# Kernel tuning notes

Measured on AMD Instinct MI355X. Metric: run time of the kernel, lower is better.

Reference implementation:

```python
import jax, jax.numpy as jnp
import numpy as np

EPS = 1e-5
N_NODES = 10
NUM_JOINTS = 6   # all robot_configs fixed to '3_segments_3DOF' (module's fallback default)
MAX_DOF = 10


def _lin(x, w, b):
    # torch nn.Linear: y = x @ W.T + b, W is (out, in)
    return jnp.einsum('...i,oi->...o', x, w) + b


def _layernorm(x, scale, bias):
    mu = x.mean(-1, keepdims=True)
    var = x.var(-1, keepdims=True)
    return (x - mu) / jnp.sqrt(var + EPS) * scale + bias


def _forward(images, text_lengths, node_features, edge_indices, p):
    B = images.shape[0]
    # --- SimplifiedVLMBackbone ---
    y = jax.lax.conv_general_dilated(images, p['conv_w'], (2, 2), [(3, 3), (3, 3)],
                                     dimension_numbers=('NCHW', 'OIHW', 'NCHW'))
    y = jax.nn.relu(y + p['conv_b'][None, :, None, None])          # (B,32,112,112)
    y = y.reshape(B, 32, 7, 16, 7, 16).mean(axis=(3, 5))            # adaptive avg pool -> (B,32,7,7)
    y = y.reshape(B, 32 * 49)
    y = jax.nn.relu(_lin(y, p['img_fc1_w'], p['img_fc1_b']))
    img_feat = _lin(y, p['img_fc2_w'], p['img_fc2_b'])               # (B,768)
    t = p['text_emb'][jnp.clip(text_lengths, 0, 9999)]               # (B,256)
    vlm = img_feat + _lin(t, p['text_fc_w'], p['text_fc_b'])         # (B,768)

    # --- SoftArmGraphNN ---
    x = jax.nn.relu(_lin(node_features, p['enc1_w'], p['enc1_b']))
    x = _lin(x, p['enc2_w'], p['enc2_b'])                            # (B,N,64)
    src, dst = edge_indices[:, 0, :], edge_indices[:, 1, :]          # (B,E)

    def agg_fn(xi, si, di):
        # mean of neighbor (source) features per destination node; 0 if no neighbors
        g = xi[si]                                                   # (E,D)
        s = jax.ops.segment_sum(g, di, num_segments=N_NODES)
        c = jax.ops.segment_sum(jnp.ones(di.shape, xi.dtype), di, num_segments=N_NODES)
        return s / jnp.maximum(c, 1.0)[:, None]

    for i in range(3):
        residual = x
        mean_nb = jax.vmap(agg_fn)(x, src, dst)                      # (B,N,64)
        comb = jnp.concatenate([x, mean_nb], axis=-1)                # (B,N,128)
        x = _lin(comb, p['gc_w'][i], p['gc_b'][i])
        x = jax.nn.relu(_layernorm(x + residual, p['ln_scale'][i], p['ln_bias'][i]))
    graph_tokens = _lin(x, p['proj_w'], p['proj_b'])                 # (B,N,32)

    # --- AttentionPooling + dual-path fusion ---
    s = _lin(jnp.tanh(_lin(graph_tokens, p['attn1_w'], p['attn1_b'])), p['attn2_w'], p['attn2_b'])
    w = jax.nn.softmax(s, axis=1)                                    # (B,N,1)
    robot_token = jnp.sum(graph_tokens * w, axis=1)                  # (B,32) -> project? 32 vs 768 -> residual add via broadcast pad
    fused = vlm.at[:, :robot_token.shape[-1]].add(robot_token)       # global token residual into vlm features

    # --- NodeActionHead (all samples: 3seg_3DOF -> 6 joints, per-joint MLPs) ---
    comb = jnp.concatenate([
        jnp.broadcast_to(fused[:, None, :], (B, NUM_JOINTS, fused.shape[-1])),
        graph_tokens[:, :NUM_JOINTS, :]], axis=-1)                   # (B,J,800)
    h = jax.nn.relu(jnp.einsum('bjf,jhf->bjh', comb, p['head_w1']) + p['head_b1'])
    h = jax.nn.relu(jnp.einsum('bjf,jhf->bjh', h, p['head_w2']) + p['head_b2'])
    a = jnp.einsum('bjf,jhf->bjh', h, p['head_w3']) + p['head_b3']   # (B,6,16)
    a = jnp.pad(a, ((0, 0), (0, MAX_DOF - NUM_JOINTS), (0, 0)))      # pad to max_dof
    return jnp.transpose(a, (0, 2, 1))                               # (B,16,10)


def setup_inputs() -> dict:
    key = jax.random.key(0)
    ks = iter(jax.random.split(key, 64))

    def nrm(shape, scale=0.02):
        return scale * jax.random.normal(next(ks), shape, dtype=jnp.float32)

    B = 128
    inp = {
        'images': jax.random.normal(next(ks), (B, 3, 224, 224), dtype=jnp.float32),
        'text_lengths': jax.random.randint(next(ks), (B,), 0, 10000, dtype=jnp.int32),
        'node_features': jax.random.normal(next(ks), (B, N_NODES, 19), dtype=jnp.float32),
        'edge_indices': jax.random.randint(next(ks), (B, 2, 18), 0, N_NODES, dtype=jnp.int32),
        'conv_w': nrm((32, 3, 7, 7)), 'conv_b': jnp.zeros(32, jnp.float32),
        'img_fc1_w': nrm((512, 1568)), 'img_fc1_b': jnp.zeros(512, jnp.float32),
        'img_fc2_w': nrm((768, 512)), 'img_fc2_b': jnp.zeros(768, jnp.float32),
        'text_emb': nrm((10000, 256)),
        'text_fc_w': nrm((768, 256)), 'text_fc_b': jnp.zeros(768, jnp.float32),
        'enc1_w': nrm((64, 19)), 'enc1_b': jnp.zeros(64, jnp.float32),
        'enc2_w': nrm((64, 64)), 'enc2_b': jnp.zeros(64, jnp.float32),
        'gc_w': nrm((3, 64, 128)), 'gc_b': jnp.zeros((3, 64), jnp.float32),
        'ln_scale': jnp.ones((3, 64), jnp.float32), 'ln_bias': jnp.zeros((3, 64), jnp.float32),
        'proj_w': nrm((32, 64)), 'proj_b': jnp.zeros(32, jnp.float32),
        'attn1_w': nrm((16, 32)), 'attn1_b': jnp.zeros(16, jnp.float32),
        'attn2_w': nrm((1, 16)), 'attn2_b': jnp.zeros(1, jnp.float32),
        'head_w1': nrm((6, 128, 800)), 'head_b1': jnp.zeros((6, 128), jnp.float32),
        'head_w2': nrm((6, 64, 128)), 'head_b2': jnp.zeros((6, 64), jnp.float32),
        'head_w3': nrm((6, 16, 64)), 'head_b3': jnp.zeros((6, 16), jnp.float32),
    }
    return inp


def reference(images, text_lengths, node_features, edge_indices, conv_w, conv_b,
              img_fc1_w, img_fc1_b, img_fc2_w, img_fc2_b, text_emb, text_fc_w, text_fc_b,
              enc1_w, enc1_b, enc2_w, enc2_b, gc_w, gc_b, ln_scale, ln_bias,
              proj_w, proj_b, attn1_w, attn1_b, attn2_w, attn2_b,
              head_w1, head_b1, head_w2, head_b2, head_w3, head_b3):
    p = dict(conv_w=conv_w, conv_b=conv_b, img_fc1_w=img_fc1_w, img_fc1_b=img_fc1_b,
             img_fc2_w=img_fc2_w, img_fc2_b=img_fc2_b, text_emb=text_emb,
             text_fc_w=text_fc_w, text_fc_b=text_fc_b, enc1_w=enc1_w, enc1_b=enc1_b,
             enc2_w=enc2_w, enc2_b=enc2_b, gc_w=gc_w, gc_b=gc_b, ln_scale=ln_scale,
             ln_bias=ln_bias, proj_w=proj_w, proj_b=proj_b, attn1_w=attn1_w,
             attn1_b=attn1_b, attn2_w=attn2_w, attn2_b=attn2_b, head_w1=head_w1,
             head_b1=head_b1, head_w2=head_w2, head_b2=head_b2, head_w3=head_w3,
             head_b3=head_b3)
    return _forward(images, text_lengths, node_features, edge_indices, p)
```

## Files before the change

### kernel.cpp

```cpp
#include <hip/hip_runtime.h>
#include <hip/hip_bf16.h>
#include <math.h>

typedef __attribute__((ext_vector_type(8))) short bf16x8;
typedef __attribute__((ext_vector_type(4))) float f32x4;

static __device__ __forceinline__ unsigned short f2bf(float f) {
    union { float f; unsigned int u; } x{f};
    unsigned int u = x.u;
    unsigned int r = (u + 0x7fffu + ((u >> 16) & 1u)) >> 16;
    return (unsigned short)r;
}

static __device__ __forceinline__ unsigned int pack2(float f0, float f1) {
    __hip_bfloat162 h = __float22bfloat162_rn(float2{f0, f1});
    union { __hip_bfloat162 h; unsigned int u; } c{h};
    return c.u;
}

__global__ __launch_bounds__(256) void wprep(const float* __restrict__ conv_w,
                                             unsigned short* __restrict__ wB) {
    for (int idx = threadIdx.x; idx < 24 * 32 * 8; idx += 256) {
        int s = idx >> 8;
        int ch = (idx >> 3) & 31;
        int kx = idx & 7;
        int c = s >> 3, ky = s & 7;
        float v = 0.f;
        if (ky < 7 && kx < 7) v = conv_w[ch * 147 + c * 49 + ky * 7 + kx];
        wB[idx] = f2bf(v);
    }
}

#define PSTRIDE 120
__global__ __launch_bounds__(512, 4) void conv_mfma(const float* __restrict__ img,
                                                    const unsigned int* __restrict__ wBu,
                                                    const float* __restrict__ cb,
                                                    float* __restrict__ pooled) {
    __shared__ unsigned int patch[111 * PSTRIDE];
    const int t = threadIdx.x;
    const int py = blockIdx.x, b = blockIdx.y;
    const int lane = t & 63, wid = t >> 6;
    const int r16 = lane & 15, g = lane >> 4;
    const int Y0 = 32 * py - 3;

    const int xc0 = 2 * lane - 3;
    const int xc1 = 2 * lane + 125;
    const int a00 = max(xc0, 0);
    const int a01 = max(xc0 + 1, 0);
    const int a10 = min(xc1, 223);
    const int a11 = min(xc1 + 1, 223);
    const bool v00 = (xc0 >= 0);
    const bool v01 = (xc0 + 1 >= 0);
    const bool v10 = (xc1 <= 223);
    const bool v11 = (xc1 + 1 <= 223);
    const bool c1act = (lane < 52);

    const float* ib = img + (size_t)b * 3 * 224 * 224;

#pragma unroll
    for (int hb = 0; hb < 2; ++hb) {
        float g0[7], g1[7], g2[7], g3[7];
        int rr[7];
        bool rv[7];
#pragma unroll
        for (int i = 0; i < 7; ++i) {
            int r = wid + 8 * (hb * 7 + i);
            int c_ = (r >= 74) ? 2 : ((r >= 37) ? 1 : 0);
            int pr = r - 37 * c_;
            int iy = Y0 + pr;
            rv[i] = (r < 111) & (iy >= 0) & (iy < 224);
            int iyc = min(max(iy, 0), 223);
            const float* rp = ib + (c_ * 224 + iyc) * 224;
            rr[i] = r;
            g0[i] = rp[a00];
            g1[i] = rp[a01];
            g2[i] = rp[a10];
            g3[i] = rp[a11];
        }
#pragma unroll
        for (int i = 0; i < 7; ++i) {
            float f0 = (rv[i] && v00) ? g0[i] : 0.f;
            float f1 = (rv[i] && v01) ? g1[i] : 0.f;
            float f2_ = (rv[i] && v10) ? g2[i] : 0.f;
            float f3 = (rv[i] && v11) ? g3[i] : 0.f;
            if (rr[i] < 111) {
                patch[rr[i] * PSTRIDE + lane] = pack2(f0, f1);
                if (c1act) patch[rr[i] * PSTRIDE + 64 + lane] = pack2(f2_, f3);
            }
        }
    }

    bf16x8 bfrA[6], bfrB[6];
    int rowoff[6];
#pragma unroll
    for (int k = 0; k < 6; ++k) {
        int s = 4 * k + g;
        int c = s >> 3, ky = s & 7;
        int kyc = ky > 6 ? 6 : ky;
        rowoff[k] = c * 37 + kyc;
        union { uint4 q; bf16x8 v; } ua, ub;
        ua.q = *(const uint4*)(wBu + (s * 32 + r16) * 4);
        ub.q = *(const uint4*)(wBu + (s * 32 + r16 + 16) * 4);
        bfrA[k] = ua.v;
        bfrB[k] = ub.v;
    }
    const float biasA = cb[r16], biasB = cb[r16 + 16];

    __syncthreads();

    float accA[7], accB[7];
#pragma unroll
    for (int p = 0; p < 7; ++p) accA[p] = accB[p] = 0.f;

#pragma unroll
    for (int q = 0; q < 2; ++q) {
        const int oyl = 2 * wid + q;
        int rb[6];
#pragma unroll
        for (int k = 0; k < 6; ++k) rb[k] = (rowoff[k] + 2 * oyl) * PSTRIDE;

        for (int t7 = 0; t7 < 7; ++t7) {
            const int oxr = 16 * t7 + r16;
            f32x4 C0 = {biasA, biasA, biasA, biasA};
            f32x4 C1 = {biasB, biasB, biasB, biasB};
#pragma unroll
            for (int k = 0; k < 6; ++k) {
                const unsigned int* ap = &patch[rb[k] + oxr];
                union { unsigned int u[4]; bf16x8 v; } ua;
                ua.u[0] = ap[0];
                ua.u[1] = ap[1];
                ua.u[2] = ap[2];
                ua.u[3] = ap[3];
                C0 = __builtin_amdgcn_mfma_f32_16x16x32_bf16(ua.v, bfrA[k], C0, 0, 0, 0);
                C1 = __builtin_amdgcn_mfma_f32_16x16x32_bf16(ua.v, bfrB[k], C1, 0, 0, 0);
            }
            float s0 = 0.f, s1 = 0.f;
#pragma unroll
            for (int r = 0; r < 4; ++r) {
                s0 += fmaxf(C0[r], 0.f);
                s1 += fmaxf(C1[r], 0.f);
            }
            accA[t7] += s0;
            accB[t7] += s1;
        }
    }
#pragma unroll
    for (int p = 0; p < 7; ++p) {
        accA[p] += __shfl_xor(accA[p], 16);
        accA[p] += __shfl_xor(accA[p], 32);
        accB[p] += __shfl_xor(accB[p], 16);
        accB[p] += __shfl_xor(accB[p], 32);
    }
    __syncthreads();
    float* sw = (float*)patch;
    if (lane < 16) {
#pragma unroll
        for (int p = 0; p < 7; ++p) {
            sw[(wid * 7 + p) * 32 + lane] = accA[p];
            sw[(wid * 7 + p) * 32 + lane + 16] = accB[p];
        }
    }
    __syncthreads();
    if (t < 224) {
        int p = t >> 5, ch = t & 31;
        float s = 0.f;
#pragma unroll
        for (int w = 0; w < 8; ++w) s += sw[(w * 7 + p) * 32 + ch];
        pooled[(size_t)b * 1568 + ch * 49 + py * 7 + p] = s * (1.f / 256.f);
    }
}

__global__ __launch_bounds__(256) void fc1_k(const float* __restrict__ in,
                                             const float* __restrict__ w,
                                             const float* __restrict__ bias,
                                             float* __restrict__ out) {
    const int t = threadIdx.x, lane = t & 63, wid = t >> 6;
    const int qg = blockIdx.x & 31;
    const int bg = blockIdx.x >> 5;
    const int b0 = bg * 8;
    const int o0 = (qg * 4 + wid) * 4;
    const float4* wp = (const float4*)w;
    const float4* xp = (const float4*)in;

    float acc[4][8];
#pragma unroll
    for (int oo = 0; oo < 4; ++oo)
#pragma unroll
        for (int r = 0; r < 8; ++r) acc[oo][r] = 0.f;

    for (int i = lane; i < 392; i += 64) {
        float4 wv[4];
#pragma unroll
        for (int oo = 0; oo < 4; ++oo) wv[oo] = wp[(size_t)(o0 + oo) * 392 + i];
#pragma unroll
        for (int r = 0; r < 8; ++r) {
            float4 xv = xp[(size_t)(b0 + r) * 392 + i];
#pragma unroll
            for (int oo = 0; oo < 4; ++oo) {
                acc[oo][r] = fmaf(xv.x, wv[oo].x, acc[oo][r]);
                acc[oo][r] = fmaf(xv.y, wv[oo].y, acc[oo][r]);
                acc[oo][r] = fmaf(xv.z, wv[oo].z, acc[oo][r]);
                acc[oo][r] = fmaf(xv.w, wv[oo].w, acc[oo][r]);
            }
        }
    }
#pragma unroll
    for (int oo = 0; oo < 4; ++oo) {
        float v = 0.f;
#pragma unroll
        for (int r = 0; r < 8; ++r) {
            float s = acc[oo][r];
            s += __shfl_xor(s, 32);
            s += __shfl_xor(s, 16);
            s += __shfl_xor(s, 8);
            s += __shfl_xor(s, 4);
            s += __shfl_xor(s, 2);
            s += __shfl_xor(s, 1);
            if (lane == r) v = s;
        }
        if (lane < 8)
            out[(size_t)(b0 + lane) * 512 + o0 + oo] = fmaxf(v + bias[o0 + oo], 0.f);
    }
}

__global__ __launch_bounds__(256) void vlm_k(const float* __restrict__ h1,
                                             const float* __restrict__ w2,
                                             const float* __restrict__ b2,
                                             const int* __restrict__ tlen,
                                             const float* __restrict__ temb,
                                             const float* __restrict__ tw,
                                             const float* __restrict__ tb,
                                             const float* __restrict__ rtok,
                                             float* __restrict__ fused) {
    const int t = threadIdx.x, lane = t & 63, wid = t >> 6;
    const int ogq = blockIdx.x % 48;
    const int bg = blockIdx.x / 48;
    const int b0 = bg * 8;
    const int o0 = (ogq * 4 + wid) * 4;

    int rows[8];
#pragma unroll
    for (int r = 0; r < 8; ++r) {
        int v = tlen[b0 + r];
        rows[r] = min(max(v, 0), 9999);
    }
    const float4* wp = (const float4*)w2;
    const float4* xp = (const float4*)h1;
    const float4* wtp = (const float4*)tw;
    const float4* xtp = (const float4*)temb;

    float acc[4][8];
#pragma unroll
    for (int oo = 0; oo < 4; ++oo)
#pragma unroll
        for (int r = 0; r < 8; ++r) acc[oo][r] = 0.f;

#pragma unroll
    for (int ii = 0; ii < 2; ++ii) {
        int i = lane + (ii << 6);
        float4 wv[4];
#pragma unroll
        for (int oo = 0; oo < 4; ++oo) wv[oo] = wp[(size_t)(o0 + oo) * 128 + i];
#pragma unroll
        for (int r = 0; r < 8; ++r) {
            float4 xv = xp[(size_t)(b0 + r) * 128 + i];
#pragma unroll
            for (int oo = 0; oo < 4; ++oo) {
                acc[oo][r] = fmaf(xv.x, wv[oo].x, acc[oo][r]);
                acc[oo][r] = fmaf(xv.y, wv[oo].y, acc[oo][r]);
                acc[oo][r] = fmaf(xv.z, wv[oo].z, acc[oo][r]);
                acc[oo][r] = fmaf(xv.w, wv[oo].w, acc[oo][r]);
            }
        }
    }
    {
        float4 wv[4];
#pragma unroll
        for (int oo = 0; oo < 4; ++oo) wv[oo] = wtp[(size_t)(o0 + oo) * 64 + lane];
#pragma unroll
        for (int r = 0; r < 8; ++r) {
            float4 xv = xtp[(size_t)rows[r] * 64 + lane];
#pragma unroll
            for (int oo = 0; oo < 4; ++oo) {
                acc[oo][r] = fmaf(xv.x, wv[oo].x, acc[oo][r]);
                acc[oo][r] = fmaf(xv.y, wv[oo].y, acc[oo][r]);
                acc[oo][r] = fmaf(xv.z, wv[oo].z, acc[oo][r]);
                acc[oo][r] = fmaf(xv.w, wv[oo].w, acc[oo][r]);
            }
        }
    }
#pragma unroll
    for (int oo = 0; oo < 4; ++oo) {
        float v = 0.f;
#pragma unroll
        for (int r = 0; r < 8; ++r) {
            float s = acc[oo][r];
            s += __shfl_xor(s, 32);
            s += __shfl_xor(s, 16);
            s += __shfl_xor(s, 8);
            s += __shfl_xor(s, 4);
            s += __shfl_xor(s, 2);
            s += __shfl_xor(s, 1);
            if (lane == r) v = s;
        }
        int o = o0 + oo;
        if (lane < 8) {
            float add = (o < 32) ? rtok[(size_t)(b0 + lane) * 32 + o] : 0.f;
            fused[(size_t)(b0 + lane) * 768 + o] = v + b2[o] + tb[o] + add;
        }
    }
}

__global__ __launch_bounds__(640, 1) void graph_k(
    const float* __restrict__ nfeat, const int* __restrict__ eidx,
    const float* __restrict__ e1w, const float* __restrict__ e1b,
    const float* __restrict__ e2w, const float* __restrict__ e2b,
    const float* __restrict__ gcw, const float* __restrict__ gcb,
    const float* __restrict__ lns, const float* __restrict__ lnb,
    const float* __restrict__ pjw, const float* __restrict__ pjb,
    const float* __restrict__ a1w, const float* __restrict__ a1b,
    const float* __restrict__ a2w, const float* __restrict__ a2b,
    float* __restrict__ gts_g, float* __restrict__ rtok) {
    __shared__ __align__(16) float pool[8448];
    __shared__ __align__(16) float nf[10][20];
    __shared__ __align__(16) float xsA[10][64];
    __shared__ __align__(16) float xsB[10][64];
    __shared__ __align__(16) float nbs[10][64];
    __shared__ __align__(16) float gtss[10][32];
    __shared__ float svs[10];
    __shared__ int se[18], de[18];
    const int t = threadIdx.x;
    const int b = blockIdx.x;
    const int n = t >> 6, o = t & 63;

    if (t < 190) {
        int nn = t / 19, i = t - nn * 19;
        nf[nn][i] = nfeat[(size_t)(b * 10 + nn) * 19 + i];
    }
    if (t < 36) {
        if (t < 18) se[t] = eidx[b * 36 + t];
        else de[t - 18] = eidx[b * 36 + t];
    }
    float* e1wT = pool;
    float* e2wT = pool + 1280;
    for (int u = t; u < 1216; u += 640) {
        int oo = u / 19, k = u - oo * 19;
        e1wT[k * 64 + oo] = e1w[u];
    }
    for (int u = t; u < 4096; u += 640) {
        int oo = u >> 6, k = u & 63;
        e2wT[k * 65 + oo] = e2w[u];
    }
    __syncthreads();

    {
        float acc = e1b[o];
#pragma unroll
        for (int i = 0; i < 19; ++i) acc = fmaf(nf[n][i], e1wT[i * 64 + o], acc);
        xsB[n][o] = fmaxf(acc, 0.f);
    }
    {
        const float* xrow = &xsB[n][0];
        float s0 = 0, s1 = 0, s2 = 0, s3 = 0;
#pragma unroll
        for (int k = 0; k < 64; k += 4) {
            s0 = fmaf(xrow[k], e2wT[k * 65 + o], s0);
            s1 = fmaf(xrow[k + 1], e2wT[(k + 1) * 65 + o], s1);
            s2 = fmaf(xrow[k + 2], e2wT[(k + 2) * 65 + o], s2);
            s3 = fmaf(xrow[k + 3], e2wT[(k + 3) * 65 + o], s3);
        }
        xsA[n][o] = e2b[o] + ((s0 + s1) + (s2 + s3));
    }
    __syncthreads();

    float* src = &xsA[0][0];
    float* dst = &xsB[0][0];
    for (int l = 0; l < 3; ++l) {
        const float* gl = gcw + (size_t)l * 8192;
        for (int u = t; u < 8192; u += 640) {
            int oo = u >> 7, k = u & 127;
            pool[k * 65 + oo] = gl[u];
        }
        {
            float s = 0.f;
            int cnt = 0;
#pragma unroll
            for (int e = 0; e < 18; ++e) {
                bool m = (de[e] == n);
                float v = src[se[e] * 64 + o];
                s += m ? v : 0.f;
                cnt += m ? 1 : 0;
            }
            nbs[n][o] = s / (float)(cnt > 1 ? cnt : 1);
        }
        __syncthreads();
        {
            const float* xa = src + n * 64;
            const float* xb = &nbs[n][0];
            float s0 = 0, s1 = 0, s2 = 0, s3 = 0;
#pragma unroll
            for (int k = 0; k < 64; k += 4) {
                s0 = fmaf(xa[k], pool[k * 65 + o], s0);
                s1 = fmaf(xa[k + 1], pool[(k + 1) * 65 + o], s1);
                s2 = fmaf(xa[k + 2], pool[(k + 2) * 65 + o], s2);
                s3 = fmaf(xa[k + 3], pool[(k + 3) * 65 + o], s3);
            }
#pragma unroll
            for (int k = 0; k < 64; k += 4) {
                s0 = fmaf(xb[k], pool[(64 + k) * 65 + o], s0);
                s1 = fmaf(xb[k + 1], pool[(64 + k + 1) * 65 + o], s1);
                s2 = fmaf(xb[k + 2], pool[(64 + k + 2) * 65 + o], s2);
                s3 = fmaf(xb[k + 3], pool[(64 + k + 3) * 65 + o], s3);
            }
            float v = gcb[l * 64 + o] + ((s0 + s1) + (s2 + s3)) + xa[o];
            float mu = v;
            mu += __shfl_xor(mu, 32);
            mu += __shfl_xor(mu, 16);
            mu += __shfl_xor(mu, 8);
            mu += __shfl_xor(mu, 4);
            mu += __shfl_xor(mu, 2);
            mu += __shfl_xor(mu, 1);
            mu *= (1.f / 64.f);
            float d = v - mu;
            float vr = d * d;
            vr += __shfl_xor(vr, 32);
            vr += __shfl_xor(vr, 16);
            vr += __shfl_xor(vr, 8);
            vr += __shfl_xor(vr, 4);
            vr += __shfl_xor(vr, 2);
            vr += __shfl_xor(vr, 1);
            vr *= (1.f / 64.f);
            dst[n * 64 + o] =
                fmaxf(d / sqrtf(vr + 1e-5f) * lns[l * 64 + o] + lnb[l * 64 + o], 0.f);
        }
        __syncthreads();
        float* tmp = src;
        src = dst;
        dst = tmp;
    }

    float* pjwT = pool;
    float* a1wT = pool + 2112;
    for (int u = t; u < 2048; u += 640) {
        int oo = u >> 6, k = u & 63;
        pjwT[k * 33 + oo] = pjw[u];
    }
    for (int u = t; u < 512; u += 640) {
        int hh = u >> 5, k = u & 31;
        a1wT[k * 17 + hh] = a1w[u];
    }
    __syncthreads();

    if (o < 32) {
        const float* xrow = src + n * 64;
        float s0 = 0, s1 = 0, s2 = 0, s3 = 0;
#pragma unroll
        for (int k = 0; k < 64; k += 4) {
            s0 = fmaf(xrow[k], pjwT[k * 33 + o], s0);
            s1 = fmaf(xrow[k + 1], pjwT[(k + 1) * 33 + o], s1);
            s2 = fmaf(xrow[k + 2], pjwT[(k + 2) * 33 + o], s2);
            s3 = fmaf(xrow[k + 3], pjwT[(k + 3) * 33 + o], s3);
        }
        float gv = pjb[o] + ((s0 + s1) + (s2 + s3));
        gtss[n][o] = gv;
        gts_g[(size_t)b * 320 + n * 32 + o] = gv;
    }
    if (o < 16) {
        const float* xrow = &gtss[n][0];
        float s0 = 0, s1 = 0, s2 = 0, s3 = 0;
#pragma unroll
        for (int k = 0; k < 32; k += 4) {
            s0 = fmaf(xrow[k], a1wT[k * 17 + o], s0);
            s1 = fmaf(xrow[k + 1], a1wT[(k + 1) * 17 + o], s1);
            s2 = fmaf(xrow[k + 2], a1wT[(k + 2) * 17 + o], s2);
            s3 = fmaf(xrow[k + 3], a1wT[(k + 3) * 17 + o], s3);
        }
        float z = a1b[o] + ((s0 + s1) + (s2 + s3));
        float sc = tanhf(z) * a2w[o];
        sc += __shfl_xor(sc, 8);
        sc += __shfl_xor(sc, 4);
        sc += __shfl_xor(sc, 2);
        sc += __shfl_xor(sc, 1);
        if (o == 0) svs[n] = sc + a2b[0];
    }
    __syncthreads();

    if (n == 0 && o < 32) {
        float m = svs[0];
#pragma unroll
        for (int i = 1; i < 10; ++i) m = fmaxf(m, svs[i]);
        float e[10];
        float sum = 0.f;
#pragma unroll
        for (int i = 0; i < 10; ++i) {
            e[i] = expf(svs[i] - m);
            sum += e[i];
        }
        float inv = 1.f / sum;
        float rt = 0.f;
#pragma unroll
        for (int nn = 0; nn < 10; ++nn) rt = fmaf(gtss[nn][o], e[nn] * inv, rt);
        rtok[(size_t)b * 32 + o] = rt;
    }
}

__global__ __launch_bounds__(256) void head1_k(const float* __restrict__ fused,
                                               const float* __restrict__ gts,
                                               const float* __restrict__ w1,
                                               const float* __restrict__ b1,
                                               float* __restrict__ h1T) {
    const int t = threadIdx.x, lane = t & 63, wid = t >> 6;
    const int ogq = blockIdx.x % 48;
    const int bg = blockIdx.x / 48;
    const int b0 = bg * 8;
    const int j = ogq >> 3;
    const int o0 = ogq * 16 + wid * 4;
    const float4* wp = (const float4*)w1;
    const float4* fp = (const float4*)fused;
    const float4* gp = (const float4*)gts;

    float acc[4][8];
#pragma unroll
    for (int oo = 0; oo < 4; ++oo)
#pragma unroll
        for (int r = 0; r < 8; ++r) acc[oo][r] = 0.f;

    for (int i = lane; i < 200; i += 64) {
        float4 wv[4];
#pragma unroll
        for (int oo = 0; oo < 4; ++oo) wv[oo] = wp[(size_t)(o0 + oo) * 200 + i];
#pragma unroll
        for (int r = 0; r < 8; ++r) {
            float4 xv = (i < 192) ? fp[(size_t)(b0 + r) * 192 + i]
                                  : gp[(size_t)(b0 + r) * 80 + j * 8 + (i - 192)];
#pragma unroll
            for (int oo = 0; oo < 4; ++oo) {
                acc[oo][r] = fmaf(xv.x, wv[oo].x, acc[oo][r]);
                acc[oo][r] = fmaf(xv.y, wv[oo].y, acc[oo][r]);
                acc[oo][r] = fmaf(xv.z, wv[oo].z, acc[oo][r]);
                acc[oo][r] = fmaf(xv.w, wv[oo].w, acc[oo][r]);
            }
        }
    }
#pragma unroll
    for (int oo = 0; oo < 4; ++oo) {
        float v = 0.f;
#pragma unroll
        for (int r = 0; r < 8; ++r) {
            float s = acc[oo][r];
            s += __shfl_xor(s, 32);
            s += __shfl_xor(s, 16);
            s += __shfl_xor(s, 8);
            s += __shfl_xor(s, 4);
            s += __shfl_xor(s, 2);
            s += __shfl_xor(s, 1);
// ... 37 lines not shown
    out[(size_t)b * 160 + oo * 10 + jj] = acc;
}

extern "C" void kernel_launch(void* const* d_in, const int* in_sizes, int n_in,
                              void* d_out, int out_size, void* d_ws, size_t ws_size,
                              hipStream_t stream) {
    const float* images = (const float*)d_in[0];
    const int* tlen = (const int*)d_in[1];
    const float* nfeat = (const float*)d_in[2];
    const int* eidx = (const int*)d_in[3];
    const float* conv_w = (const float*)d_in[4];
    const float* conv_b = (const float*)d_in[5];
    const float* fc1w = (const float*)d_in[6];
    const float* fc1b = (const float*)d_in[7];
    const float* fc2w = (const float*)d_in[8];
    const float* fc2b = (const float*)d_in[9];
    const float* temb = (const float*)d_in[10];
    const float* tfw = (const float*)d_in[11];
    const float* tfb = (const float*)d_in[12];
    const float* e1w = (const float*)d_in[13];
    const float* e1b = (const float*)d_in[14];
    const float* e2w = (const float*)d_in[15];
    const float* e2b = (const float*)d_in[16];
    const float* gcw = (const float*)d_in[17];
    const float* gcb = (const float*)d_in[18];
    const float* lns = (const float*)d_in[19];
    const float* lnb = (const float*)d_in[20];
    const float* pjw = (const float*)d_in[21];
    const float* pjb = (const float*)d_in[22];
    const float* a1w = (const float*)d_in[23];
    const float* a1b = (const float*)d_in[24];
    const float* a2w = (const float*)d_in[25];
    const float* a2b = (const float*)d_in[26];
    const float* w1 = (const float*)d_in[27];
    const float* b1 = (const float*)d_in[28];
    const float* w2 = (const float*)d_in[29];
    const float* b2 = (const float*)d_in[30];
    const float* w3 = (const float*)d_in[31];
    const float* b3 = (const float*)d_in[32];

    const int B = in_sizes[0] / (3 * 224 * 224);

    float* ws = (float*)d_ws;
    unsigned short* wB = (unsigned short*)d_ws;
    float* pooled = ws + 3072;
    float* h1fc = pooled + (size_t)B * 1568;
    float* fused = h1fc + (size_t)B * 512;
    float* gts = fused + (size_t)B * 768;
    float* rtok = gts + (size_t)B * 320;
    float* h1T = pooled;
    float* h2T = pooled + 98304;

    wprep<<<1, 256, 0, stream>>>(conv_w, wB);
    conv_mfma<<<dim3(7, B), 512, 0, stream>>>(images, (const unsigned int*)wB,
                                              conv_b, pooled);
    fc1_k<<<512, 256, 0, stream>>>(pooled, fc1w, fc1b, h1fc);
    graph_k<<<B, 640, 0, stream>>>(nfeat, eidx, e1w, e1b, e2w, e2b, gcw, gcb,
                                   lns, lnb, pjw, pjb, a1w, a1b, a2w, a2b,
                                   gts, rtok);
    vlm_k<<<768, 256, 0, stream>>>(h1fc, fc2w, fc2b, tlen, temb, tfw, tfb,
                                   rtok, fused);
    head1_k<<<768, 256, 0, stream>>>(fused, gts, w1, b1, h1T);
    head2_k<<<384, 128, 0, stream>>>(h1T, w2, b2, h2T);
    head3_k<<<160, 128, 0, stream>>>(h2T, w3, b3, (float*)d_out);
}
```

Measured before the change: 119.9 us.

## Merge graph network kernel into conv kernel as extra block column

The graph network work is folded into the convolution launch as an eighth block per batch row, so a separate kernel launch goes away and the graph work runs alongside the conv blocks. Shared memory is now one union buffer sized for the conv patch, and the graph code is reworked to use 512 threads (8 waves looping over 10 nodes) instead of 640. This saves a launch and overlaps the small graph work with conv, but the graph blocks now run with fewer threads and under the conv kernel's launch bounds.

```diff
diff --git a/kernel.cpp b/kernel.cpp
--- a/kernel.cpp
+++ b/kernel.cpp
@@ -32,286 +32,9 @@
 }
 
 #define PSTRIDE 120
-__global__ __launch_bounds__(512, 4) void conv_mfma(const float* __restrict__ img,
-                                                    const unsigned int* __restrict__ wBu,
-                                                    const float* __restrict__ cb,
-                                                    float* __restrict__ pooled) {
-    __shared__ unsigned int patch[111 * PSTRIDE];
-    const int t = threadIdx.x;
-    const int py = blockIdx.x, b = blockIdx.y;
-    const int lane = t & 63, wid = t >> 6;
-    const int r16 = lane & 15, g = lane >> 4;
-    const int Y0 = 32 * py - 3;
-
-    const int xc0 = 2 * lane - 3;
-    const int xc1 = 2 * lane + 125;
-    const int a00 = max(xc0, 0);
-    const int a01 = max(xc0 + 1, 0);
-    const int a10 = min(xc1, 223);
-    const int a11 = min(xc1 + 1, 223);
-    const bool v00 = (xc0 >= 0);
-    const bool v01 = (xc0 + 1 >= 0);
-    const bool v10 = (xc1 <= 223);
-    const bool v11 = (xc1 + 1 <= 223);
-    const bool c1act = (lane < 52);
-
-    const float* ib = img + (size_t)b * 3 * 224 * 224;
-
-#pragma unroll
-    for (int hb = 0; hb < 2; ++hb) {
-        float g0[7], g1[7], g2[7], g3[7];
-        int rr[7];
-        bool rv[7];
-#pragma unroll
-        for (int i = 0; i < 7; ++i) {
-            int r = wid + 8 * (hb * 7 + i);
-            int c_ = (r >= 74) ? 2 : ((r >= 37) ? 1 : 0);
-            int pr = r - 37 * c_;
-            int iy = Y0 + pr;
-            rv[i] = (r < 111) & (iy >= 0) & (iy < 224);
-            int iyc = min(max(iy, 0), 223);
-            const float* rp = ib + (c_ * 224 + iyc) * 224;
-            rr[i] = r;
-            g0[i] = rp[a00];
-            g1[i] = rp[a01];
-            g2[i] = rp[a10];
-            g3[i] = rp[a11];
-        }
-#pragma unroll
-        for (int i = 0; i < 7; ++i) {
-            float f0 = (rv[i] && v00) ? g0[i] : 0.f;
-            float f1 = (rv[i] && v01) ? g1[i] : 0.f;
-            float f2_ = (rv[i] && v10) ? g2[i] : 0.f;
-            float f3 = (rv[i] && v11) ? g3[i] : 0.f;
-            if (rr[i] < 111) {
-                patch[rr[i] * PSTRIDE + lane] = pack2(f0, f1);
-                if (c1act) patch[rr[i] * PSTRIDE + 64 + lane] = pack2(f2_, f3);
-            }
-        }
-    }
-
-    bf16x8 bfrA[6], bfrB[6];
-    int rowoff[6];
-#pragma unroll
-    for (int k = 0; k < 6; ++k) {
-        int s = 4 * k + g;
-        int c = s >> 3, ky = s & 7;
-        int kyc = ky > 6 ? 6 : ky;
-        rowoff[k] = c * 37 + kyc;
-        union { uint4 q; bf16x8 v; } ua, ub;
-        ua.q = *(const uint4*)(wBu + (s * 32 + r16) * 4);
-        ub.q = *(const uint4*)(wBu + (s * 32 + r16 + 16) * 4);
-        bfrA[k] = ua.v;
-        bfrB[k] = ub.v;
-    }
-    const float biasA = cb[r16], biasB = cb[r16 + 16];
-
-    __syncthreads();
-
-    float accA[7], accB[7];
-#pragma unroll
-    for (int p = 0; p < 7; ++p) accA[p] = accB[p] = 0.f;
-
-#pragma unroll
-    for (int q = 0; q < 2; ++q) {
-        const int oyl = 2 * wid + q;
-        int rb[6];
-#pragma unroll
-        for (int k = 0; k < 6; ++k) rb[k] = (rowoff[k] + 2 * oyl) * PSTRIDE;
-
-        for (int t7 = 0; t7 < 7; ++t7) {
-            const int oxr = 16 * t7 + r16;
-            f32x4 C0 = {biasA, biasA, biasA, biasA};
-            f32x4 C1 = {biasB, biasB, biasB, biasB};
-#pragma unroll
-            for (int k = 0; k < 6; ++k) {
-                const unsigned int* ap = &patch[rb[k] + oxr];
-                union { unsigned int u[4]; bf16x8 v; } ua;
-                ua.u[0] = ap[0];
-                ua.u[1] = ap[1];
-                ua.u[2] = ap[2];
-                ua.u[3] = ap[3];
-                C0 = __builtin_amdgcn_mfma_f32_16x16x32_bf16(ua.v, bfrA[k], C0, 0, 0, 0);
-                C1 = __builtin_amdgcn_mfma_f32_16x16x32_bf16(ua.v, bfrB[k], C1, 0, 0, 0);
-            }
-            float s0 = 0.f, s1 = 0.f;
-#pragma unroll
-            for (int r = 0; r < 4; ++r) {
-                s0 += fmaxf(C0[r], 0.f);
-                s1 += fmaxf(C1[r], 0.f);
-            }
-            accA[t7] += s0;
-            accB[t7] += s1;
-        }
-    }
-#pragma unroll
-    for (int p = 0; p < 7; ++p) {
-        accA[p] += __shfl_xor(accA[p], 16);
-        accA[p] += __shfl_xor(accA[p], 32);
-        accB[p] += __shfl_xor(accB[p], 16);
-        accB[p] += __shfl_xor(accB[p], 32);
-    }
-    __syncthreads();
-    float* sw = (float*)patch;
-    if (lane < 16) {
-#pragma unroll
-        for (int p = 0; p < 7; ++p) {
-            sw[(wid * 7 + p) * 32 + lane] = accA[p];
-            sw[(wid * 7 + p) * 32 + lane + 16] = accB[p];
-        }
-    }
-    __syncthreads();
-    if (t < 224) {
-        int p = t >> 5, ch = t & 31;
-        float s = 0.f;
-#pragma unroll
-        for (int w = 0; w < 8; ++w) s += sw[(w * 7 + p) * 32 + ch];
-        pooled[(size_t)b * 1568 + ch * 49 + py * 7 + p] = s * (1.f / 256.f);
-    }
-}
-
-__global__ __launch_bounds__(256) void fc1_k(const float* __restrict__ in,
-                                             const float* __restrict__ w,
-                                             const float* __restrict__ bias,
-                                             float* __restrict__ out) {
-    const int t = threadIdx.x, lane = t & 63, wid = t >> 6;
-    const int qg = blockIdx.x & 31;
-    const int bg = blockIdx.x >> 5;
-    const int b0 = bg * 8;
-    const int o0 = (qg * 4 + wid) * 4;
-    const float4* wp = (const float4*)w;
-    const float4* xp = (const float4*)in;
-
-    float acc[4][8];
-#pragma unroll
-    for (int oo = 0; oo < 4; ++oo)
-#pragma unroll
-        for (int r = 0; r < 8; ++r) acc[oo][r] = 0.f;
-
-    for (int i = lane; i < 392; i += 64) {
-        float4 wv[4];
-#pragma unroll
-        for (int oo = 0; oo < 4; ++oo) wv[oo] = wp[(size_t)(o0 + oo) * 392 + i];
-#pragma unroll
-        for (int r = 0; r < 8; ++r) {
-            float4 xv = xp[(size_t)(b0 + r) * 392 + i];
-#pragma unroll
-            for (int oo = 0; oo < 4; ++oo) {
-                acc[oo][r] = fmaf(xv.x, wv[oo].x, acc[oo][r]);
-                acc[oo][r] = fmaf(xv.y, wv[oo].y, acc[oo][r]);
-                acc[oo][r] = fmaf(xv.z, wv[oo].z, acc[oo][r]);
-                acc[oo][r] = fmaf(xv.w, wv[oo].w, acc[oo][r]);
-            }
-        }
-    }
-#pragma unroll
-    for (int oo = 0; oo < 4; ++oo) {
-        float v = 0.f;
-#pragma unroll
-        for (int r = 0; r < 8; ++r) {
-            float s = acc[oo][r];
-            s += __shfl_xor(s, 32);
-            s += __shfl_xor(s, 16);
-            s += __shfl_xor(s, 8);
-            s += __shfl_xor(s, 4);
-            s += __shfl_xor(s, 2);
-            s += __shfl_xor(s, 1);
-            if (lane == r) v = s;
-        }
-        if (lane < 8)
-            out[(size_t)(b0 + lane) * 512 + o0 + oo] = fmaxf(v + bias[o0 + oo], 0.f);
-    }
-}
-
-__global__ __launch_bounds__(256) void vlm_k(const float* __restrict__ h1,
-                                             const float* __restrict__ w2,
-                                             const float* __restrict__ b2,
-                                             const int* __restrict__ tlen,
-                                             const float* __restrict__ temb,
-                                             const float* __restrict__ tw,
-                                             const float* __restrict__ tb,
-                                             const float* __restrict__ rtok,
-                                             float* __restrict__ fused) {
-    const int t = threadIdx.x, lane = t & 63, wid = t >> 6;
-    const int ogq = blockIdx.x % 48;
-    const int bg = blockIdx.x / 48;
-    const int b0 = bg * 8;
-    const int o0 = (ogq * 4 + wid) * 4;
-
-    int rows[8];
-#pragma unroll
-    for (int r = 0; r < 8; ++r) {
-        int v = tlen[b0 + r];
-        rows[r] = min(max(v, 0), 9999);
-    }
-    const float4* wp = (const float4*)w2;
-    const float4* xp = (const float4*)h1;
-    const float4* wtp = (const float4*)tw;
-    const float4* xtp = (const float4*)temb;
-
-    float acc[4][8];
-#pragma unroll
-    for (int oo = 0; oo < 4; ++oo)
-#pragma unroll
-        for (int r = 0; r < 8; ++r) acc[oo][r] = 0.f;
-
-#pragma unroll
-    for (int ii = 0; ii < 2; ++ii) {
-        int i = lane + (ii << 6);
-        float4 wv[4];
-#pragma unroll
-        for (int oo = 0; oo < 4; ++oo) wv[oo] = wp[(size_t)(o0 + oo) * 128 + i];
-#pragma unroll
-        for (int r = 0; r < 8; ++r) {
-            float4 xv = xp[(size_t)(b0 + r) * 128 + i];
-#pragma unroll
-            for (int oo = 0; oo < 4; ++oo) {
-                acc[oo][r] = fmaf(xv.x, wv[oo].x, acc[oo][r]);
-                acc[oo][r] = fmaf(xv.y, wv[oo].y, acc[oo][r]);
-                acc[oo][r] = fmaf(xv.z, wv[oo].z, acc[oo][r]);
-                acc[oo][r] = fmaf(xv.w, wv[oo].w, acc[oo][r]);
-            }
-        }
-    }
-    {
-        float4 wv[4];
-#pragma unroll
-        for (int oo = 0; oo < 4; ++oo) wv[oo] = wtp[(size_t)(o0 + oo) * 64 + lane];
-#pragma unroll
-        for (int r = 0; r < 8; ++r) {
-            float4 xv = xtp[(size_t)rows[r] * 64 + lane];
-#pragma unroll
-            for (int oo = 0; oo < 4; ++oo) {
-                acc[oo][r] = fmaf(xv.x, wv[oo].x, acc[oo][r]);
-                acc[oo][r] = fmaf(xv.y, wv[oo].y, acc[oo][r]);
-                acc[oo][r] = fmaf(xv.z, wv[oo].z, acc[oo][r]);
-                acc[oo][r] = fmaf(xv.w, wv[oo].w, acc[oo][r]);
-            }
-        }
-    }
-#pragma unroll
-    for (int oo = 0; oo < 4; ++oo) {
-        float v = 0.f;
-#pragma unroll
-        for (int r = 0; r < 8; ++r) {
-            float s = acc[oo][r];
-            s += __shfl_xor(s, 32);
-            s += __shfl_xor(s, 16);
-            s += __shfl_xor(s, 8);
-            s += __shfl_xor(s, 4);
-            s += __shfl_xor(s, 2);
-            s += __shfl_xor(s, 1);
-            if (lane == r) v = s;
-        }
-        int o = o0 + oo;
-        if (lane < 8) {
-            float add = (o < 32) ? rtok[(size_t)(b0 + lane) * 32 + o] : 0.f;
-            fused[(size_t)(b0 + lane) * 768 + o] = v + b2[o] + tb[o] + add;
-        }
-    }
-}
-
-__global__ __launch_bounds__(640, 1) void graph_k(
+__global__ __launch_bounds__(512, 4) void conv_graph(
+    const float* __restrict__ img, const unsigned int* __restrict__ wBu,
+    const float* __restrict__ cb, float* __restrict__ pooled,
     const float* __restrict__ nfeat, const int* __restrict__ eidx,
     const float* __restrict__ e1w, const float* __restrict__ e1b,
     const float* __restrict__ e2w, const float* __restrict__ e2b,
@@ -321,98 +44,234 @@
     const float* __restrict__ a1w, const float* __restrict__ a1b,
     const float* __restrict__ a2w, const float* __restrict__ a2b,
     float* __restrict__ gts_g, float* __restrict__ rtok) {
-    __shared__ __align__(16) float pool[8448];
-    __shared__ __align__(16) float nf[10][20];
-    __shared__ __align__(16) float xsA[10][64];
-    __shared__ __align__(16) float xsB[10][64];
-    __shared__ __align__(16) float nbs[10][64];
-    __shared__ __align__(16) float gtss[10][32];
-    __shared__ float svs[10];
-    __shared__ int se[18], de[18];
+    __shared__ __align__(16) unsigned int smem_u[111 * PSTRIDE];
     const int t = threadIdx.x;
-    const int b = blockIdx.x;
-    const int n = t >> 6, o = t & 63;
+    const int b = blockIdx.y;
+    const int lane = t & 63, wid = t >> 6;
+
+    if (blockIdx.x < 7) {
+        unsigned int* patch = smem_u;
+        const int py = blockIdx.x;
+        const int r16 = lane & 15, g = lane >> 4;
+        const int Y0 = 32 * py - 3;
+
+        const int xc0 = 2 * lane - 3;
+        const int xc1 = 2 * lane + 125;
+        const int a00 = max(xc0, 0);
+        const int a01 = max(xc0 + 1, 0);
+        const int a10 = min(xc1, 223);
+        const int a11 = min(xc1 + 1, 223);
+        const bool v00 = (xc0 >= 0);
+        const bool v01 = (xc0 + 1 >= 0);
+        const bool v10 = (xc1 <= 223);
+        const bool v11 = (xc1 + 1 <= 223);
+        const bool c1act = (lane < 52);
+
+        const float* ib = img + (size_t)b * 3 * 224 * 224;
+
+#pragma unroll
+        for (int hb = 0; hb < 2; ++hb) {
+            float g0[7], g1[7], g2[7], g3[7];
+            int rr[7];
+            bool rv[7];
+#pragma unroll
+            for (int i = 0; i < 7; ++i) {
+                int r = wid + 8 * (hb * 7 + i);
+                int c_ = (r >= 74) ? 2 : ((r >= 37) ? 1 : 0);
+                int pr = r - 37 * c_;
+                int iy = Y0 + pr;
+                rv[i] = (r < 111) & (iy >= 0) & (iy < 224);
+                int iyc = min(max(iy, 0), 223);
+                const float* rp = ib + (c_ * 224 + iyc) * 224;
+                rr[i] = r;
+                g0[i] = rp[a00];
+                g1[i] = rp[a01];
+                g2[i] = rp[a10];
+                g3[i] = rp[a11];
+            }
+#pragma unroll
+            for (int i = 0; i < 7; ++i) {
+                float f0 = (rv[i] && v00) ? g0[i] : 0.f;
+                float f1 = (rv[i] && v01) ? g1[i] : 0.f;
+                float f2_ = (rv[i] && v10) ? g2[i] : 0.f;
+                float f3 = (rv[i] && v11) ? g3[i] : 0.f;
+                if (rr[i] < 111) {
+                    patch[rr[i] * PSTRIDE + lane] = pack2(f0, f1);
+                    if (c1act) patch[rr[i] * PSTRIDE + 64 + lane] = pack2(f2_, f3);
+                }
+            }
+        }
+
+        bf16x8 bfrA[6], bfrB[6];
+        int rowoff[6];
+#pragma unroll
+        for (int k = 0; k < 6; ++k) {
+            int s = 4 * k + g;
+            int c = s >> 3, ky = s & 7;
+            int kyc = ky > 6 ? 6 : ky;
+            rowoff[k] = c * 37 + kyc;
+            union { uint4 q; bf16x8 v; } ua, ub;
+            ua.q = *(const uint4*)(wBu + (s * 32 + r16) * 4);
+            ub.q = *(const uint4*)(wBu + (s * 32 + r16 + 16) * 4);
+            bfrA[k] = ua.v;
+            bfrB[k] = ub.v;
+        }
+        const float biasA = cb[r16], biasB = cb[r16 + 16];
+
+        __syncthreads();
+
+        float accA[7], accB[7];
+#pragma unroll
+        for (int p = 0; p < 7; ++p) accA[p] = accB[p] = 0.f;
+
+#pragma unroll
+        for (int q = 0; q < 2; ++q) {
+            const int oyl = 2 * wid + q;
+            int rb[6];
+#pragma unroll
+            for (int k = 0; k < 6; ++k) rb[k] = (rowoff[k] + 2 * oyl) * PSTRIDE;
+
+            for (int t7 = 0; t7 < 7; ++t7) {
+                const int oxr = 16 * t7 + r16;
+                f32x4 C0 = {biasA, biasA, biasA, biasA};
+                f32x4 C1 = {biasB, biasB, biasB, biasB};
+#pragma unroll
+                for (int k = 0; k < 6; ++k) {
+                    const unsigned int* ap = &patch[rb[k] + oxr];
+                    union { unsigned int u[4]; bf16x8 v; } ua;
+                    ua.u[0] = ap[0];
+                    ua.u[1] = ap[1];
+                    ua.u[2] = ap[2];
+                    ua.u[3] = ap[3];
+                    C0 = __builtin_amdgcn_mfma_f32_16x16x32_bf16(ua.v, bfrA[k], C0, 0, 0, 0);
+                    C1 = __builtin_amdgcn_mfma_f32_16x16x32_bf16(ua.v, bfrB[k], C1, 0, 0, 0);
+                }
+                float s0 = 0.f, s1 = 0.f;
+#pragma unroll
+                for (int r = 0; r < 4; ++r) {
+                    s0 += fmaxf(C0[r], 0.f);
+                    s1 += fmaxf(C1[r], 0.f);
+                }
+                accA[t7] += s0;
+                accB[t7] += s1;
+            }
+        }
+#pragma unroll
+        for (int p = 0; p < 7; ++p) {
+            accA[p] += __shfl_xor(accA[p], 16);
+            accA[p] += __shfl_xor(accA[p], 32);
+            accB[p] += __shfl_xor(accB[p], 16);
+            accB[p] += __shfl_xor(accB[p], 32);
+        }
+        __syncthreads();
+        float* sw = (float*)smem_u;
+        if (lane < 16) {
+#pragma unroll
+            for (int p = 0; p < 7; ++p) {
+                sw[(wid * 7 + p) * 32 + lane] = accA[p];
+                sw[(wid * 7 + p) * 32 + lane + 16] = accB[p];
+            }
+        }
+        __syncthreads();
+        if (t < 224) {
+            int p = t >> 5, ch = t & 31;
+            float s = 0.f;
+#pragma unroll
+            for (int w = 0; w < 8; ++w) s += sw[(w * 7 + p) * 32 + ch];
+            pooled[(size_t)b * 1568 + ch * 49 + py * 7 + p] = s * (1.f / 256.f);
+        }
+        return;
+    }
+
+    float* fbase = (float*)smem_u;
+    float* gpool = fbase;
+    float* nf = gpool + 8448;
+    float* xsA = nf + 200;
+    float* xsB = xsA + 640;
+    float* nbs = xsB + 640;
+    float* gtss = nbs + 640;
+    float* svs = gtss + 320;
+    int* se = (int*)(svs + 12);
+    int* de = se + 18;
 
     if (t < 190) {
         int nn = t / 19, i = t - nn * 19;
-        nf[nn][i] = nfeat[(size_t)(b * 10 + nn) * 19 + i];
+        nf[nn * 20 + i] = nfeat[(size_t)(b * 10 + nn) * 19 + i];
     }
     if (t < 36) {
         if (t < 18) se[t] = eidx[b * 36 + t];
         else de[t - 18] = eidx[b * 36 + t];
     }
-    float* e1wT = pool;
-    float* e2wT = pool + 1280;
-    for (int u = t; u < 1216; u += 640) {
+    float* e1wT = gpool;
+    float* e2wT = gpool + 1280;
+    for (int u = t; u < 1216; u += 512) {
         int oo = u / 19, k = u - oo * 19;
         e1wT[k * 64 + oo] = e1w[u];
     }
-    for (int u = t; u < 4096; u += 640) {
+    for (int u = t; u < 4096; u += 512) {
         int oo = u >> 6, k = u & 63;
         e2wT[k * 65 + oo] = e2w[u];
     }
     __syncthreads();
 
-    {
-        float acc = e1b[o];
-#pragma unroll
-        for (int i = 0; i < 19; ++i) acc = fmaf(nf[n][i], e1wT[i * 64 + o], acc);
-        xsB[n][o] = fmaxf(acc, 0.f);
-    }
-    {
-        const float* xrow = &xsB[n][0];
+    for (int n2 = wid; n2 < 10; n2 += 8) {
+        float acc = e1b[lane];
+#pragma unroll
+        for (int i = 0; i < 19; ++i) acc = fmaf(nf[n2 * 20 + i], e1wT[i * 64 + lane], acc);
+        xsB[n2 * 64 + lane] = fmaxf(acc, 0.f);
+        const float* xrow = &xsB[n2 * 64];
         float s0 = 0, s1 = 0, s2 = 0, s3 = 0;
 #pragma unroll
         for (int k = 0; k < 64; k += 4) {
-            s0 = fmaf(xrow[k], e2wT[k * 65 + o], s0);
-            s1 = fmaf(xrow[k + 1], e2wT[(k + 1) * 65 + o], s1);
-            s2 = fmaf(xrow[k + 2], e2wT[(k + 2) * 65 + o], s2);
-            s3 = fmaf(xrow[k + 3], e2wT[(k + 3) * 65 + o], s3);
-        }
-        xsA[n][o] = e2b[o] + ((s0 + s1) + (s2 + s3));
+            s0 = fmaf(xrow[k], e2wT[k * 65 + lane], s0);
+            s1 = fmaf(xrow[k + 1], e2wT[(k + 1) * 65 + lane], s1);
+            s2 = fmaf(xrow[k + 2], e2wT[(k + 2) * 65 + lane], s2);
+            s3 = fmaf(xrow[k + 3], e2wT[(k + 3) * 65 + lane], s3);
+        }
+        xsA[n2 * 64 + lane] = e2b[lane] + ((s0 + s1) + (s2 + s3));
     }
     __syncthreads();
 
-    float* src = &xsA[0][0];
-    float* dst = &xsB[0][0];
+    float* src = xsA;
+    float* dst = xsB;
     for (int l = 0; l < 3; ++l) {
         const float* gl = gcw + (size_t)l * 8192;
-        for (int u = t; u < 8192; u += 640) {
+        for (int u = t; u < 8192; u += 512) {
             int oo = u >> 7, k = u & 127;
-            pool[k * 65 + oo] = gl[u];
-        }
-        {
+            gpool[k * 65 + oo] = gl[u];
+        }
+        for (int n2 = wid; n2 < 10; n2 += 8) {
             float s = 0.f;
             int cnt = 0;
 #pragma unroll
             for (int e = 0; e < 18; ++e) {
-                bool m = (de[e] == n);
-                float v = src[se[e] * 64 + o];
+                bool m = (de[e] == n2);
+                float v = src[se[e] * 64 + lane];
                 s += m ? v : 0.f;
                 cnt += m ? 1 : 0;
             }
-            nbs[n][o] = s / (float)(cnt > 1 ? cnt : 1);
+            nbs[n2 * 64 + lane] = s / (float)(cnt > 1 ? cnt : 1);
         }
         __syncthreads();
-        {
-            const float* xa = src + n * 64;
-            const float* xb = &nbs[n][0];
+        for (int n2 = wid; n2 < 10; n2 += 8) {
+            const float* xa = src + n2 * 64;
+            const float* xb = nbs + n2 * 64;
             float s0 = 0, s1 = 0, s2 = 0, s3 = 0;
 #pragma unroll
             for (int k = 0; k < 64; k += 4) {
-                s0 = fmaf(xa[k], pool[k * 65 + o], s0);
-                s1 = fmaf(xa[k + 1], pool[(k + 1) * 65 + o], s1);
-                s2 = fmaf(xa[k + 2], pool[(k + 2) * 65 + o], s2);
-                s3 = fmaf(xa[k + 3], pool[(k + 3) * 65 + o], s3);
+                s0 = fmaf(xa[k], gpool[k * 65 + lane], s0);
+                s1 = fmaf(xa[k + 1], gpool[(k + 1) * 65 + lane], s1);
+                s2 = fmaf(xa[k + 2], gpool[(k + 2) * 65 + lane], s2);
+                s3 = fmaf(xa[k + 3], gpool[(k + 3) * 65 + lane], s3);
             }
 #pragma unroll
             for (int k = 0; k < 64; k += 4) {
-                s0 = fmaf(xb[k], pool[(64 + k) * 65 + o], s0);
-                s1 = fmaf(xb[k + 1], pool[(64 + k + 1) * 65 + o], s1);
-                s2 = fmaf(xb[k + 2], pool[(64 + k + 2) * 65 + o], s2);
-                s3 = fmaf(xb[k + 3], pool[(64 + k + 3) * 65 + o], s3);
-            }
-            float v = gcb[l * 64 + o] + ((s0 + s1) + (s2 + s3)) + xa[o];
+                s0 = fmaf(xb[k], gpool[(64 + k) * 65 + lane], s0);
+                s1 = fmaf(xb[k + 1], gpool[(64 + k + 1) * 65 + lane], s1);
+                s2 = fmaf(xb[k + 2], gpool[(64 + k + 2) * 65 + lane], s2);
+                s3 = fmaf(xb[k + 3], gpool[(64 + k + 3) * 65 + lane], s3);
+            }
+            float v = gcb[l * 64 + lane] + ((s0 + s1) + (s2 + s3)) + xa[lane];
             float mu = v;
             mu += __shfl_xor(mu, 32);
             mu += __shfl_xor(mu, 16);
@@ -430,8 +289,8 @@
             vr += __shfl_xor(vr, 2);
             vr += __shfl_xor(vr, 1);
             vr *= (1.f / 64.f);
-            dst[n * 64 + o] =
-                fmaxf(d / sqrtf(vr + 1e-5f) * lns[l * 64 + o] + lnb[l * 64 + o], 0.f);
+            dst[n2 * 64 + lane] =
+                fmaxf(d / sqrtf(vr + 1e-5f) * lns[l * 64 + lane] + lnb[l * 64 + lane], 0.f);
         }
         __syncthreads();
         float* tmp = src;
@@ -439,53 +298,56 @@
         dst = tmp;
     }
 
-    float* pjwT = pool;
-    float* a1wT = pool + 2112;
-    for (int u = t; u < 2048; u += 640) {
+    float* pjwT = gpool;
+    float* a1wT = gpool + 2112;
+    for (int u = t; u < 2048; u += 512) {
         int oo = u >> 6, k = u & 63;
         pjwT[k * 33 + oo] = pjw[u];
     }
-    for (int u = t; u < 512; u += 640) {
+    if (t < 512) {
+        int u = t;
         int hh = u >> 5, k = u & 31;
         a1wT[k * 17 + hh] = a1w[u];
     }
     __syncthreads();
 
-    if (o < 32) {
-        const float* xrow = src + n * 64;
-        float s0 = 0, s1 = 0, s2 = 0, s3 = 0;
-#pragma unroll
-        for (int k = 0; k < 64; k += 4) {
-            s0 = fmaf(xrow[k], pjwT[k * 33 + o], s0);
-            s1 = fmaf(xrow[k + 1], pjwT[(k + 1) * 33 + o], s1);
-            s2 = fmaf(xrow[k + 2], pjwT[(k + 2) * 33 + o], s2);
-            s3 = fmaf(xrow[k + 3], pjwT[(k + 3) * 33 + o], s3);
-        }
-        float gv = pjb[o] + ((s0 + s1) + (s2 + s3));
-        gtss[n][o] = gv;
-        gts_g[(size_t)b * 320 + n * 32 + o] = gv;
-    }
-    if (o < 16) {
-        const float* xrow = &gtss[n][0];
-        float s0 = 0, s1 = 0, s2 = 0, s3 = 0;
-#pragma unroll
-        for (int k = 0; k < 32; k += 4) {
-            s0 = fmaf(xrow[k], a1wT[k * 17 + o], s0);
-            s1 = fmaf(xrow[k + 1], a1wT[(k + 1) * 17 + o], s1);
-            s2 = fmaf(xrow[k + 2], a1wT[(k + 2) * 17 + o], s2);
-            s3 = fmaf(xrow[k + 3], a1wT[(k + 3) * 17 + o], s3);
-        }
-        float z = a1b[o] + ((s0 + s1) + (s2 + s3));
-        float sc = tanhf(z) * a2w[o];
-        sc += __shfl_xor(sc, 8);
-        sc += __shfl_xor(sc, 4);
-        sc += __shfl_xor(sc, 2);
-        sc += __shfl_xor(sc, 1);
-        if (o == 0) svs[n] = sc + a2b[0];
+    for (int n2 = wid; n2 < 10; n2 += 8) {
+        if (lane < 32) {
+            const float* xrow = src + n2 * 64;
+            float s0 = 0, s1 = 0, s2 = 0, s3 = 0;
+#pragma unroll
+            for (int k = 0; k < 64; k += 4) {
+                s0 = fmaf(xrow[k], pjwT[k * 33 + lane], s0);
+                s1 = fmaf(xrow[k + 1], pjwT[(k + 1) * 33 + lane], s1);
+                s2 = fmaf(xrow[k + 2], pjwT[(k + 2) * 33 + lane], s2);
+                s3 = fmaf(xrow[k + 3], pjwT[(k + 3) * 33 + lane], s3);
+            }
+            float gv = pjb[lane] + ((s0 + s1) + (s2 + s3));
+            gtss[n2 * 32 + lane] = gv;
+            gts_g[(size_t)b * 320 + n2 * 32 + lane] = gv;
+        }
+        if (lane < 16) {
+            const float* xrow = gtss + n2 * 32;
+            float s0 = 0, s1 = 0, s2 = 0, s3 = 0;
+#pragma unroll
+            for (int k = 0; k < 32; k += 4) {
+                s0 = fmaf(xrow[k], a1wT[k * 17 + lane], s0);
+                s1 = fmaf(xrow[k + 1], a1wT[(k + 1) * 17 + lane], s1);
+                s2 = fmaf(xrow[k + 2], a1wT[(k + 2) * 17 + lane], s2);
+                s3 = fmaf(xrow[k + 3], a1wT[(k + 3) * 17 + lane], s3);
+            }
+            float z = a1b[lane] + ((s0 + s1) + (s2 + s3));
+            float sc = tanhf(z) * a2w[lane];
+            sc += __shfl_xor(sc, 8);
+            sc += __shfl_xor(sc, 4);
+            sc += __shfl_xor(sc, 2);
+            sc += __shfl_xor(sc, 1);
+            if (lane == 0) svs[n2] = sc + a2b[0];
+        }
     }
     __syncthreads();
 
-    if (n == 0 && o < 32) {
+    if (wid == 0 && lane < 32) {
         float m = svs[0];
 #pragma unroll
         for (int i = 1; i < 10; ++i) m = fmaxf(m, svs[i]);
@@ -499,8 +361,149 @@
         float inv = 1.f / sum;
         float rt = 0.f;
 #pragma unroll
-        for (int nn = 0; nn < 10; ++nn) rt = fmaf(gtss[nn][o], e[nn] * inv, rt);
-        rtok[(size_t)b * 32 + o] = rt;
+        for (int nn = 0; nn < 10; ++nn) rt = fmaf(gtss[nn * 32 + lane], e[nn] * inv, rt);
+        rtok[(size_t)b * 32 + lane] = rt;
+    }
+}
+
+__global__ __launch_bounds__(256) void fc1_k(const float* __restrict__ in,
+                                             const float* __restrict__ w,
+                                             const float* __restrict__ bias,
+                                             float* __restrict__ out) {
+    const int t = threadIdx.x, lane = t & 63, wid = t >> 6;
+    const int qg = blockIdx.x & 31;
+    const int bg = blockIdx.x >> 5;
+    const int b0 = bg * 8;
+    const int o0 = (qg * 4 + wid) * 4;
+    const float4* wp = (const float4*)w;
+    const float4* xp = (const float4*)in;
+
+    float acc[4][8];
+#pragma unroll
+    for (int oo = 0; oo < 4; ++oo)
+#pragma unroll
+        for (int r = 0; r < 8; ++r) acc[oo][r] = 0.f;
+
+    for (int i = lane; i < 392; i += 64) {
+        float4 wv[4];
+#pragma unroll
+        for (int oo = 0; oo < 4; ++oo) wv[oo] = wp[(size_t)(o0 + oo) * 392 + i];
+#pragma unroll
+        for (int r = 0; r < 8; ++r) {
+            float4 xv = xp[(size_t)(b0 + r) * 392 + i];
+#pragma unroll
+            for (int oo = 0; oo < 4; ++oo) {
+                acc[oo][r] = fmaf(xv.x, wv[oo].x, acc[oo][r]);
+                acc[oo][r] = fmaf(xv.y, wv[oo].y, acc[oo][r]);
+                acc[oo][r] = fmaf(xv.z, wv[oo].z, acc[oo][r]);
+                acc[oo][r] = fmaf(xv.w, wv[oo].w, acc[oo][r]);
+            }
+        }
+    }
+#pragma unroll
+    for (int oo = 0; oo < 4; ++oo) {
+        float v = 0.f;
+#pragma unroll
+        for (int r = 0; r < 8; ++r) {
+            float s = acc[oo][r];
+            s += __shfl_xor(s, 32);
+            s += __shfl_xor(s, 16);
+            s += __shfl_xor(s, 8);
+            s += __shfl_xor(s, 4);
+            s += __shfl_xor(s, 2);
+            s += __shfl_xor(s, 1);
+            if (lane == r) v = s;
+        }
+        if (lane < 8)
+            out[(size_t)(b0 + lane) * 512 + o0 + oo] = fmaxf(v + bias[o0 + oo], 0.f);
+    }
+}
+
+__global__ __launch_bounds__(256) void vlm_k(const float* __restrict__ h1,
+                                             const float* __restrict__ w2,
+                                             const float* __restrict__ b2,
+                                             const int* __restrict__ tlen,
+                                             const float* __restrict__ temb,
+                                             const float* __restrict__ tw,
+                                             const float* __restrict__ tb,
+                                             const float* __restrict__ rtok,
+                                             float* __restrict__ fused) {
+    const int t = threadIdx.x, lane = t & 63, wid = t >> 6;
+    const int ogq = blockIdx.x % 48;
+    const int bg = blockIdx.x / 48;
+    const int b0 = bg * 8;
+    const int o0 = (ogq * 4 + wid) * 4;
+
+    int rows[8];
+#pragma unroll
+    for (int r = 0; r < 8; ++r) {
+        int v = tlen[b0 + r];
+        rows[r] = min(max(v, 0), 9999);
+    }
+    const float4* wp = (const float4*)w2;
+    const float4* xp = (const float4*)h1;
+    const float4* wtp = (const float4*)tw;
+    const float4* xtp = (const float4*)temb;
+
+    float acc[4][8];
+#pragma unroll
+    for (int oo = 0; oo < 4; ++oo)
+#pragma unroll
+        for (int r = 0; r < 8; ++r) acc[oo][r] = 0.f;
+
+#pragma unroll
+    for (int ii = 0; ii < 2; ++ii) {
+        int i = lane + (ii << 6);
+        float4 wv[4];
+#pragma unroll
+        for (int oo = 0; oo < 4; ++oo) wv[oo] = wp[(size_t)(o0 + oo) * 128 + i];
+#pragma unroll
+        for (int r = 0; r < 8; ++r) {
+            float4 xv = xp[(size_t)(b0 + r) * 128 + i];
+#pragma unroll
+            for (int oo = 0; oo < 4; ++oo) {
+                acc[oo][r] = fmaf(xv.x, wv[oo].x, acc[oo][r]);
+                acc[oo][r] = fmaf(xv.y, wv[oo].y, acc[oo][r]);
+                acc[oo][r] = fmaf(xv.z, wv[oo].z, acc[oo][r]);
+                acc[oo][r] = fmaf(xv.w, wv[oo].w, acc[oo][r]);
+            }
+        }
+    }
+    {
+        float4 wv[4];
+#pragma unroll
+        for (int oo = 0; oo < 4; ++oo) wv[oo] = wtp[(size_t)(o0 + oo) * 64 + lane];
+#pragma unroll
+        for (int r = 0; r < 8; ++r) {
+            float4 xv = xtp[(size_t)rows[r] * 64 + lane];
+#pragma unroll
+            for (int oo = 0; oo < 4; ++oo) {
+                acc[oo][r] = fmaf(xv.x, wv[oo].x, acc[oo][r]);
+                acc[oo][r] = fmaf(xv.y, wv[oo].y, acc[oo][r]);
+                acc[oo][r] = fmaf(xv.z, wv[oo].z, acc[oo][r]);
+                acc[oo][r] = fmaf(xv.w, wv[oo].w, acc[oo][r]);
+            }
+        }
+    }
+#pragma unroll
+    for (int oo = 0; oo < 4; ++oo) {
+        float v = 0.f;
+#pragma unroll
+        for (int r = 0; r < 8; ++r) {
+            float s = acc[oo][r];
+            s += __shfl_xor(s, 32);
+            s += __shfl_xor(s, 16);
+            s += __shfl_xor(s, 8);
+            s += __shfl_xor(s, 4);
+            s += __shfl_xor(s, 2);
+            s += __shfl_xor(s, 1);
+            if (lane == r) v = s;
+        }
+        int o = o0 + oo;
+        if (lane < 8) {
+            float add = (o < 32) ? rtok[(size_t)(b0 + lane) * 32 + o] : 0.f;
+            fused[(size_t)(b0 + lane) * 768 + o] = v + b2[o] + tb[o] + add;
+        }
     }
 }
 
@@ -644,12 +647,11 @@
     float* h2T = pooled + 98304;
 
     wprep<<<1, 256, 0, stream>>>(conv_w, wB);
-    conv_mfma<<<dim3(7, B), 512, 0, stream>>>(images, (const unsigned int*)wB,
-                                              conv_b, pooled);
+    conv_graph<<<dim3(8, B), 512, 0, stream>>>(
+        images, (const unsigned int*)wB, conv_b, pooled,
+        nfeat, eidx, e1w, e1b, e2w, e2b, gcw, gcb, lns, lnb,
+        pjw, pjb, a1w, a1b, a2w, a2b, gts, rtok);
     fc1_k<<<512, 256, 0, stream>>>(pooled, fc1w, fc1b, h1fc);
-    graph_k<<<B, 640, 0, stream>>>(nfeat, eidx, e1w, e1b, e2w, e2b, gcw, gcb,
-                                   lns, lnb, pjw, pjb, a1w, a1b, a2w, a2b,
-                                   gts, rtok);
     vlm_k<<<768, 256, 0, stream>>>(h1fc, fc2w, fc2b, tlen, temb, tfw, tfb,
                                    rtok, fused);
     head1_k<<<768, 256, 0, stream>>>(fused, gts, w1, b1, h1T);
```

Result: slower. 182.7 us (+52.3%).
